# Performance work log

Hardware: AMD Instinct MI355X
Metric: run time of the kernel (lower is better)

## Reference

```python
import jax, jax.numpy as jnp
import numpy as np

B, T, D_MODEL, H, D = 8, 1024, 1024, 16, 64
NEG = -1.0e9

def setup_inputs() -> dict:
    key = jax.random.key(0)
    ks = jax.random.split(key, 11)
    s = 1.0 / np.sqrt(D_MODEL)
    inp = {
        'q': jax.random.normal(ks[0], (B, T, D_MODEL), jnp.float32),
        'k': jax.random.normal(ks[1], (B, T, D_MODEL), jnp.float32),
        'v': jax.random.normal(ks[2], (B, T, D_MODEL), jnp.float32),
        'Wq': jax.random.normal(ks[3], (H * D, D_MODEL), jnp.float32) * s,
        'bq': jnp.zeros((H * D,), jnp.float32),
        'Wk': jax.random.normal(ks[4], (H * D, D_MODEL), jnp.float32) * s,
        'bk': jnp.zeros((H * D,), jnp.float32),
        'Wv': jax.random.normal(ks[5], (H * D, D_MODEL), jnp.float32) * s,
        'bv': jnp.zeros((H * D,), jnp.float32),
        'Wo': jax.random.normal(ks[6], (D, H * D), jnp.float32) * (1.0 / np.sqrt(H * D)),
        'bo': jnp.zeros((D,), jnp.float32),
        'mask': jnp.ones((T, T), jnp.int32),
    }
    return inp

def reference(q, k, v, Wq, bq, Wk, bk, Wv, bv, Wo, bo, mask):
    Bn, Tq = q.shape[0], q.shape[1]
    Tk = k.shape[1]
    # QKV projections (torch Linear: y = x @ W.T + b), split heads
    qh = (q @ Wq.T + bq).reshape(Bn, Tq, H, D).transpose(0, 2, 1, 3)  # (B,H,Tq,D)
    kh = (k @ Wk.T + bk).reshape(Bn, Tk, H, D).transpose(0, 2, 1, 3)  # (B,H,Tk,D)
    vh = (v @ Wv.T + bv).reshape(Bn, Tk, H, D).transpose(0, 2, 1, 3)  # (B,H,Tk,D)
    scale = 1.0 / jnp.sqrt(jnp.asarray(D, qh.dtype))
    scores = jnp.einsum('bhqd,bhkd->bhqk', qh * scale, kh)  # (B,H,Tq,Tk)
    scores = jnp.where(mask[None, None, :, :] == 0, jnp.asarray(NEG, scores.dtype), scores)
    attn = jax.nn.softmax(scores, axis=-1)
    ctx = jnp.einsum('bhqk,bhkd->bhqd', attn, vh)  # (B,H,Tq,D)
    ctx = ctx.transpose(0, 2, 1, 3).reshape(Bn, Tq, H * D)
    out = ctx @ Wo.T + bo  # (B,Tq,D)
    return out, attn
```

## Files before the change

kernel.cpp:

```cpp
#include <hip/hip_runtime.h>

typedef __attribute__((ext_vector_type(8))) short short8;
typedef __attribute__((ext_vector_type(4))) float f32x4;

#define MFMA16(a, b, c) __builtin_amdgcn_mfma_f32_16x16x32_bf16((a), (b), (c), 0, 0, 0)

static __device__ inline unsigned short f2bf(float f) {
    unsigned int u = __float_as_uint(f);
    u += 0x7fffu + ((u >> 16) & 1u);
    return (unsigned short)(u >> 16);
}

static __device__ inline ushort4 pack4(float4 x) {
    ushort4 r;
    r.x = f2bf(x.x); r.y = f2bf(x.y); r.z = f2bf(x.z); r.w = f2bf(x.w);
    return r;
}

static __device__ inline short8 cvt8(const float* __restrict__ p) {
    float4 x = *(const float4*)p;
    float4 y = *(const float4*)(p + 4);
    short8 r;
    r[0] = (short)f2bf(x.x); r[1] = (short)f2bf(x.y); r[2] = (short)f2bf(x.z); r[3] = (short)f2bf(x.w);
    r[4] = (short)f2bf(y.x); r[5] = (short)f2bf(y.y); r[6] = (short)f2bf(y.z); r[7] = (short)f2bf(y.w);
    return r;
}

__global__ __launch_bounds__(256) void qkv_proj_kernel(
    const float* __restrict__ q, const float* __restrict__ k, const float* __restrict__ v,
    const float* __restrict__ Wq, const float* __restrict__ bq,
    const float* __restrict__ Wk, const float* __restrict__ bk,
    const float* __restrict__ Wv, const float* __restrict__ bv,
    unsigned short* __restrict__ Qh, unsigned short* __restrict__ Kh,
    unsigned short* __restrict__ Vt)
{
    __shared__ unsigned short As[128][40];
    __shared__ unsigned short Bs[128][40];

    const int z = blockIdx.z;
    const float* X    = (z == 0) ? q  : (z == 1) ? k  : v;
    const float* W    = (z == 0) ? Wq : (z == 1) ? Wk : Wv;
    const float* bias = (z == 0) ? bq : (z == 1) ? bk : bv;

    const int m0 = blockIdx.y * 128;
    const int n0 = blockIdx.x * 128;
    const int tid = threadIdx.x;
    const int w = tid >> 6, lane = tid & 63, lr = lane & 15, lg = lane >> 4;
    const int wr = w >> 1, wc = w & 1;

    f32x4 acc[4][4];
    #pragma unroll
    for (int mi = 0; mi < 4; ++mi)
        #pragma unroll
        for (int ni = 0; ni < 4; ++ni) acc[mi][ni] = (f32x4){0.f, 0.f, 0.f, 0.f};

    for (int k0 = 0; k0 < 1024; k0 += 32) {
        #pragma unroll
        for (int i = 0; i < 4; ++i) {
            int vv = tid + 256 * i;
            int row = vv >> 3, c4 = vv & 7;
            float4 xa = *(const float4*)(X + (size_t)(m0 + row) * 1024 + k0 + c4 * 4);
            float4 xb = *(const float4*)(W + (size_t)(n0 + row) * 1024 + k0 + c4 * 4);
            *(ushort4*)&As[row][c4 * 4] = pack4(xa);
            *(ushort4*)&Bs[row][c4 * 4] = pack4(xb);
        }
        __syncthreads();
        short8 a[4], bf[4];
        #pragma unroll
        for (int mi = 0; mi < 4; ++mi) a[mi]  = *(const short8*)&As[wr * 64 + mi * 16 + lr][lg * 8];
        #pragma unroll
        for (int ni = 0; ni < 4; ++ni) bf[ni] = *(const short8*)&Bs[wc * 64 + ni * 16 + lr][lg * 8];
        #pragma unroll
        for (int mi = 0; mi < 4; ++mi)
            #pragma unroll
            for (int ni = 0; ni < 4; ++ni)
                acc[mi][ni] = MFMA16(a[mi], bf[ni], acc[mi][ni]);
        __syncthreads();
    }

    #pragma unroll
    for (int ni = 0; ni < 4; ++ni) {
        int n = n0 + wc * 64 + ni * 16 + lr;
        float bb = bias[n];
        int h = n >> 6, d = n & 63;
        #pragma unroll
        for (int mi = 0; mi < 4; ++mi) {
            #pragma unroll
            for (int r = 0; r < 4; ++r) {
                int m = m0 + wr * 64 + mi * 16 + lg * 4 + r;
                float val = acc[mi][ni][r] + bb;
                int bi = m >> 10, t = m & 1023;
                size_t hb = ((size_t)(bi * 16 + h)) << 16;
                if (z == 0)      Qh[hb + (size_t)t * 64 + d] = f2bf(val);
                else if (z == 1) Kh[hb + (size_t)t * 64 + d] = f2bf(val);
                else             Vt[hb + (size_t)d * 1024 + t] = f2bf(val);
            }
        }
    }
}

__global__ __launch_bounds__(256) void attn_kernel(
    const unsigned short* __restrict__ Qh, const unsigned short* __restrict__ Kh,
    const unsigned short* __restrict__ Vt, const int* __restrict__ mask,
    float* __restrict__ attn, unsigned short* __restrict__ ctx)
{
    __shared__ unsigned short pb[16][1032];
    __shared__ float redA[16][4];
    __shared__ float redB[16][4];

    const int qt = blockIdx.x;
    const int bh = blockIdx.y;
    const int tid = threadIdx.x;
    const int w = tid >> 6, lane = tid & 63, lr = lane & 15, lg = lane >> 4;
    const int qrow0 = qt * 16;

    const unsigned short* Qbase = Qh + ((size_t)bh << 16) + (size_t)qrow0 * 64;
    short8 aq0 = *(const short8*)(Qbase + (size_t)lr * 64 + lg * 8);
    short8 aq1 = *(const short8*)(Qbase + (size_t)lr * 64 + 32 + lg * 8);

    f32x4 acc[16];
    const unsigned short* Kbase = Kh + ((size_t)bh << 16) + (size_t)(w * 256) * 64;
    #pragma unroll
    for (int nt = 0; nt < 16; ++nt) {
        f32x4 c = {0.f, 0.f, 0.f, 0.f};
        const unsigned short* kp = Kbase + (size_t)(nt * 16 + lr) * 64 + lg * 8;
        short8 b0 = *(const short8*)kp;
        short8 b1 = *(const short8*)(kp + 32);
        c = MFMA16(aq0, b0, c);
        c = MFMA16(aq1, b1, c);
        acc[nt] = c;
    }

    #pragma unroll
    for (int nt = 0; nt < 16; ++nt) {
        int kcol = w * 256 + nt * 16 + lr;
        #pragma unroll
        for (int r = 0; r < 4; ++r) {
            int qr = lg * 4 + r;
            float s = acc[nt][r] * 0.125f;
            int mv = mask[(size_t)(qrow0 + qr) * 1024 + kcol];
            acc[nt][r] = (mv == 0) ? -1.0e9f : s;
        }
    }

    float pm[4];
    #pragma unroll
    for (int r = 0; r < 4; ++r) {
        float m_ = -3.4e38f;
        #pragma unroll
        for (int nt = 0; nt < 16; ++nt) m_ = fmaxf(m_, acc[nt][r]);
        pm[r] = m_;
    }
    #pragma unroll
    for (int off = 1; off < 16; off <<= 1) {
        #pragma unroll
        for (int r = 0; r < 4; ++r) pm[r] = fmaxf(pm[r], __shfl_xor(pm[r], off));
    }
    if (lr < 4) redA[lg * 4 + lr][w] = pm[lr];
    __syncthreads();
    float rowm[4];
    #pragma unroll
    for (int r = 0; r < 4; ++r)
        rowm[r] = fmaxf(fmaxf(redA[lg * 4 + r][0], redA[lg * 4 + r][1]),
                        fmaxf(redA[lg * 4 + r][2], redA[lg * 4 + r][3]));

    float ps[4] = {0.f, 0.f, 0.f, 0.f};
    #pragma unroll
    for (int nt = 0; nt < 16; ++nt) {
        #pragma unroll
        for (int r = 0; r < 4; ++r) {
            float p = __expf(acc[nt][r] - rowm[r]);
            acc[nt][r] = p;
            ps[r] += p;
        }
    }
    #pragma unroll
    for (int off = 1; off < 16; off <<= 1) {
        #pragma unroll
        for (int r = 0; r < 4; ++r) ps[r] += __shfl_xor(ps[r], off);
    }
    if (lr < 4) redB[lg * 4 + lr][w] = ps[lr];
    __syncthreads();
    float inv[4];
    #pragma unroll
    for (int r = 0; r < 4; ++r) {
        float s = (redB[lg * 4 + r][0] + redB[lg * 4 + r][1]) +
                  (redB[lg * 4 + r][2] + redB[lg * 4 + r][3]);
        inv[r] = 1.0f / s;
    }

    float* arow = attn + ((size_t)bh << 20) + (size_t)qrow0 * 1024;
    #pragma unroll
    for (int nt = 0; nt < 16; ++nt) {
        int kcol = w * 256 + nt * 16 + lr;
        #pragma unroll
        for (int r = 0; r < 4; ++r) {
            int qr = lg * 4 + r;
            float a = acc[nt][r] * inv[r];
            arow[(size_t)qr * 1024 + kcol] = a;
            pb[qr][kcol] = f2bf(a);
        }
    }
    __syncthreads();

    f32x4 co = {0.f, 0.f, 0.f, 0.f};
    const unsigned short* Vbase = Vt + ((size_t)bh << 16) + (size_t)(w * 16) * 1024;
    #pragma unroll 8
    for (int ks = 0; ks < 32; ++ks) {
        short8 ap = *(const short8*)&pb[lr][ks * 32 + lg * 8];
        short8 bv_ = *(const short8*)(Vbase + (size_t)lr * 1024 + ks * 32 + lg * 8);
        co = MFMA16(ap, bv_, co);
    }
    unsigned short* cb = ctx + ((size_t)(bh >> 4) * 1024 + qrow0) * 1024 + (size_t)(bh & 15) * 64;
    #pragma unroll
    for (int r = 0; r < 4; ++r)
        cb[(size_t)(lg * 4 + r) * 1024 + w * 16 + lr] = f2bf(co[r]);
}

__global__ __launch_bounds__(256) void oproj_kernel(
    const unsigned short* __restrict__ ctx, const float* __restrict__ Wo,
    const float* __restrict__ bo, float* __restrict__ out)
{
    const int m0 = blockIdx.x * 64;
    const int tid = threadIdx.x;
    const int w = tid >> 6, lane = tid & 63, lr = lane & 15, lg = lane >> 4;

    f32x4 acc[4];
    #pragma unroll
    for (int i = 0; i < 4; ++i) acc[i] = (f32x4){0.f, 0.f, 0.f, 0.f};

    const unsigned short* abase = ctx + (size_t)(m0 + w * 16 + lr) * 1024 + lg * 8;
    #pragma unroll 4
    for (int ks = 0; ks < 32; ++ks) {
        short8 a = *(const short8*)(abase + (size_t)ks * 32);
        #pragma unroll
        for (int nt = 0; nt < 4; ++nt) {
            short8 b = cvt8(Wo + (size_t)(nt * 16 + lr) * 1024 + ks * 32 + lg * 8);
            acc[nt] = MFMA16(a, b, acc[nt]);
        }
    }
    #pragma unroll
    for (int nt = 0; nt < 4; ++nt) {
        int n = nt * 16 + lr;
        float bb = bo[n];
        #pragma unroll
        for (int r = 0; r < 4; ++r) {
            int m = m0 + w * 16 + lg * 4 + r;
            out[(size_t)m * 64 + n] = acc[nt][r] + bb;
        }
    }
}

extern "C" void kernel_launch(void* const* d_in, const int* in_sizes, int n_in,
                              void* d_out, int out_size, void* d_ws, size_t ws_size,
                              hipStream_t stream)
{
    (void)in_sizes; (void)n_in; (void)out_size; (void)ws_size;

    const float* q  = (const float*)d_in[0];
    const float* k  = (const float*)d_in[1];
    const float* v  = (const float*)d_in[2];
    const float* Wq = (const float*)d_in[3];
    const float* bq = (const float*)d_in[4];
    const float* Wk = (const float*)d_in[5];
    const float* bk = (const float*)d_in[6];
    const float* Wv = (const float*)d_in[7];
    const float* bv = (const float*)d_in[8];
    const float* Wo = (const float*)d_in[9];
    const float* bo = (const float*)d_in[10];
    const int* mask = (const int*)d_in[11];

    float* out  = (float*)d_out;
    float* attn = out + (size_t)8 * 1024 * 64;

    unsigned short* Qh  = (unsigned short*)d_ws;
    unsigned short* Kh  = Qh + (size_t)8388608;
    unsigned short* Vt  = Kh + (size_t)8388608;
    unsigned short* ctx = Vt + (size_t)8388608;

    qkv_proj_kernel<<<dim3(8, 64, 3), 256, 0, stream>>>(q, k, v, Wq, bq, Wk, bk, Wv, bv, Qh, Kh, Vt);
    attn_kernel<<<dim3(64, 128), 256, 0, stream>>>(Qh, Kh, Vt, mask, attn, ctx);
    oproj_kernel<<<dim3(128), 256, 0, stream>>>(ctx, Wo, bo, out);
}
```

Measured before the change: 1.060 ms.

## Transpose QK^T MFMA so each lane owns a row; vectorize attn stores and mask loads

```diff
diff --git a/kernel.cpp b/kernel.cpp
--- a/kernel.cpp
+++ b/kernel.cpp
@@ -14,15 +14,6 @@
 static __device__ inline ushort4 pack4(float4 x) {
     ushort4 r;
     r.x = f2bf(x.x); r.y = f2bf(x.y); r.z = f2bf(x.z); r.w = f2bf(x.w);
-    return r;
-}
-
-static __device__ inline short8 cvt8(const float* __restrict__ p) {
-    float4 x = *(const float4*)p;
-    float4 y = *(const float4*)(p + 4);
-    short8 r;
-    r[0] = (short)f2bf(x.x); r[1] = (short)f2bf(x.y); r[2] = (short)f2bf(x.z); r[3] = (short)f2bf(x.w);
-    r[4] = (short)f2bf(y.x); r[5] = (short)f2bf(y.y); r[6] = (short)f2bf(y.z); r[7] = (short)f2bf(y.w);
     return r;
 }
 
@@ -104,7 +95,7 @@
     const unsigned short* __restrict__ Vt, const int* __restrict__ mask,
     float* __restrict__ attn, unsigned short* __restrict__ ctx)
 {
-    __shared__ unsigned short pb[16][1032];
+    __shared__ unsigned short pb[16][1040];
     __shared__ float redA[16][4];
     __shared__ float redB[16][4];
 
@@ -115,8 +106,8 @@
     const int qrow0 = qt * 16;
 
     const unsigned short* Qbase = Qh + ((size_t)bh << 16) + (size_t)qrow0 * 64;
-    short8 aq0 = *(const short8*)(Qbase + (size_t)lr * 64 + lg * 8);
-    short8 aq1 = *(const short8*)(Qbase + (size_t)lr * 64 + 32 + lg * 8);
+    short8 bq0 = *(const short8*)(Qbase + (size_t)lr * 64 + lg * 8);
+    short8 bq1 = *(const short8*)(Qbase + (size_t)lr * 64 + 32 + lg * 8);
 
     f32x4 acc[16];
     const unsigned short* Kbase = Kh + ((size_t)bh << 16) + (size_t)(w * 256) * 64;
@@ -124,82 +115,59 @@
     for (int nt = 0; nt < 16; ++nt) {
         f32x4 c = {0.f, 0.f, 0.f, 0.f};
         const unsigned short* kp = Kbase + (size_t)(nt * 16 + lr) * 64 + lg * 8;
-        short8 b0 = *(const short8*)kp;
-        short8 b1 = *(const short8*)(kp + 32);
-        c = MFMA16(aq0, b0, c);
-        c = MFMA16(aq1, b1, c);
+        short8 k0 = *(const short8*)kp;
+        short8 k1 = *(const short8*)(kp + 32);
+        c = MFMA16(k0, bq0, c);
+        c = MFMA16(k1, bq1, c);
         acc[nt] = c;
     }
 
-    #pragma unroll
-    for (int nt = 0; nt < 16; ++nt) {
-        int kcol = w * 256 + nt * 16 + lr;
+    const int qr = qrow0 + lr;
+    const int colbase = w * 256 + lg * 4;
+    const int* mrow = mask + (size_t)qr * 1024 + colbase;
+
+    float pm = -3.4e38f;
+    #pragma unroll
+    for (int nt = 0; nt < 16; ++nt) {
+        int4 mv = *(const int4*)(mrow + nt * 16);
+        float s0 = acc[nt][0] * 0.125f, s1 = acc[nt][1] * 0.125f;
+        float s2 = acc[nt][2] * 0.125f, s3 = acc[nt][3] * 0.125f;
+        acc[nt][0] = (mv.x == 0) ? -1.0e9f : s0;
+        acc[nt][1] = (mv.y == 0) ? -1.0e9f : s1;
+        acc[nt][2] = (mv.z == 0) ? -1.0e9f : s2;
+        acc[nt][3] = (mv.w == 0) ? -1.0e9f : s3;
+        pm = fmaxf(pm, fmaxf(fmaxf(acc[nt][0], acc[nt][1]), fmaxf(acc[nt][2], acc[nt][3])));
+    }
+    pm = fmaxf(pm, __shfl_xor(pm, 16));
+    pm = fmaxf(pm, __shfl_xor(pm, 32));
+    if (lg == 0) redA[lr][w] = pm;
+    __syncthreads();
+    float rowm = fmaxf(fmaxf(redA[lr][0], redA[lr][1]), fmaxf(redA[lr][2], redA[lr][3]));
+
+    float ps = 0.f;
+    #pragma unroll
+    for (int nt = 0; nt < 16; ++nt) {
         #pragma unroll
         for (int r = 0; r < 4; ++r) {
-            int qr = lg * 4 + r;
-            float s = acc[nt][r] * 0.125f;
-            int mv = mask[(size_t)(qrow0 + qr) * 1024 + kcol];
-            acc[nt][r] = (mv == 0) ? -1.0e9f : s;
-        }
-    }
-
-    float pm[4];
-    #pragma unroll
-    for (int r = 0; r < 4; ++r) {
-        float m_ = -3.4e38f;
-        #pragma unroll
-        for (int nt = 0; nt < 16; ++nt) m_ = fmaxf(m_, acc[nt][r]);
-        pm[r] = m_;
-    }
-    #pragma unroll
-    for (int off = 1; off < 16; off <<= 1) {
-        #pragma unroll
-        for (int r = 0; r < 4; ++r) pm[r] = fmaxf(pm[r], __shfl_xor(pm[r], off));
-    }
-    if (lr < 4) redA[lg * 4 + lr][w] = pm[lr];
+            float p = __expf(acc[nt][r] - rowm);
+            acc[nt][r] = p;
+            ps += p;
+        }
+    }
+    ps += __shfl_xor(ps, 16);
+    ps += __shfl_xor(ps, 32);
+    if (lg == 0) redB[lr][w] = ps;
     __syncthreads();
-    float rowm[4];
-    #pragma unroll
-    for (int r = 0; r < 4; ++r)
-        rowm[r] = fmaxf(fmaxf(redA[lg * 4 + r][0], redA[lg * 4 + r][1]),
-                        fmaxf(redA[lg * 4 + r][2], redA[lg * 4 + r][3]));
-
-    float ps[4] = {0.f, 0.f, 0.f, 0.f};
-    #pragma unroll
-    for (int nt = 0; nt < 16; ++nt) {
-        #pragma unroll
-        for (int r = 0; r < 4; ++r) {
-            float p = __expf(acc[nt][r] - rowm[r]);
-            acc[nt][r] = p;
-            ps[r] += p;
-        }
-    }
-    #pragma unroll
-    for (int off = 1; off < 16; off <<= 1) {
-        #pragma unroll
-        for (int r = 0; r < 4; ++r) ps[r] += __shfl_xor(ps[r], off);
-    }
-    if (lr < 4) redB[lg * 4 + lr][w] = ps[lr];
-    __syncthreads();
-    float inv[4];
-    #pragma unroll
-    for (int r = 0; r < 4; ++r) {
-        float s = (redB[lg * 4 + r][0] + redB[lg * 4 + r][1]) +
-                  (redB[lg * 4 + r][2] + redB[lg * 4 + r][3]);
-        inv[r] = 1.0f / s;
-    }
-
-    float* arow = attn + ((size_t)bh << 20) + (size_t)qrow0 * 1024;
-    #pragma unroll
-    for (int nt = 0; nt < 16; ++nt) {
-        int kcol = w * 256 + nt * 16 + lr;
-        #pragma unroll
-        for (int r = 0; r < 4; ++r) {
-            int qr = lg * 4 + r;
-            float a = acc[nt][r] * inv[r];
-            arow[(size_t)qr * 1024 + kcol] = a;
-            pb[qr][kcol] = f2bf(a);
-        }
+    float inv = 1.0f / ((redB[lr][0] + redB[lr][1]) + (redB[lr][2] + redB[lr][3]));
+
+    float* arow = attn + ((size_t)bh << 20) + (size_t)qr * 1024 + colbase;
+    #pragma unroll
+    for (int nt = 0; nt < 16; ++nt) {
+        float4 av;
+        av.x = acc[nt][0] * inv; av.y = acc[nt][1] * inv;
+        av.z = acc[nt][2] * inv; av.w = acc[nt][3] * inv;
+        *(float4*)(arow + nt * 16) = av;
+        *(ushort4*)&pb[lr][colbase + nt * 16] = pack4(av);
     }
     __syncthreads();
 
@@ -207,7 +175,7 @@
     const unsigned short* Vbase = Vt + ((size_t)bh << 16) + (size_t)(w * 16) * 1024;
     #pragma unroll 8
     for (int ks = 0; ks < 32; ++ks) {
-        short8 ap = *(const short8*)&pb[lr][ks * 32 + lg * 8];
+        short8 ap  = *(const short8*)&pb[lr][ks * 32 + lg * 8];
         short8 bv_ = *(const short8*)(Vbase + (size_t)lr * 1024 + ks * 32 + lg * 8);
         co = MFMA16(ap, bv_, co);
     }
@@ -217,8 +185,16 @@
         cb[(size_t)(lg * 4 + r) * 1024 + w * 16 + lr] = f2bf(co[r]);
 }
 
+__global__ __launch_bounds__(256) void wo_cvt_kernel(
+    const float* __restrict__ Wo, unsigned short* __restrict__ wob)
+{
+    int i = (blockIdx.x * 256 + threadIdx.x) * 4;
+    float4 x = *(const float4*)(Wo + i);
+    *(ushort4*)(wob + i) = pack4(x);
+}
+
 __global__ __launch_bounds__(256) void oproj_kernel(
-    const unsigned short* __restrict__ ctx, const float* __restrict__ Wo,
+    const unsigned short* __restrict__ ctx, const unsigned short* __restrict__ wob,
     const float* __restrict__ bo, float* __restrict__ out)
 {
     const int m0 = blockIdx.x * 64;
@@ -235,7 +211,7 @@
         short8 a = *(const short8*)(abase + (size_t)ks * 32);
         #pragma unroll
         for (int nt = 0; nt < 4; ++nt) {
-            short8 b = cvt8(Wo + (size_t)(nt * 16 + lr) * 1024 + ks * 32 + lg * 8);
+            short8 b = *(const short8*)(wob + (size_t)(nt * 16 + lr) * 1024 + ks * 32 + lg * 8);
             acc[nt] = MFMA16(a, b, acc[nt]);
         }
     }
@@ -277,8 +253,10 @@
     unsigned short* Kh  = Qh + (size_t)8388608;
     unsigned short* Vt  = Kh + (size_t)8388608;
     unsigned short* ctx = Vt + (size_t)8388608;
+    unsigned short* wob = Qh;
 
     qkv_proj_kernel<<<dim3(8, 64, 3), 256, 0, stream>>>(q, k, v, Wq, bq, Wk, bk, Wv, bv, Qh, Kh, Vt);
     attn_kernel<<<dim3(64, 128), 256, 0, stream>>>(Qh, Kh, Vt, mask, attn, ctx);
-    oproj_kernel<<<dim3(128), 256, 0, stream>>>(ctx, Wo, bo, out);
-}
+    wo_cvt_kernel<<<dim3(64), 256, 0, stream>>>(Wo, wob);
+    oproj_kernel<<<dim3(128), 256, 0, stream>>>(ctx, wob, bo, out);
+}
```

Measured after the change: 1.118 ms. 5.5% more time.
